# Kernel tuning notes

Hardware: AMD Instinct MI355X
Metric: run time of the kernel (lower is better)

Reference implementation:

```python
import jax, jax.numpy as jnp
import numpy as np

# ---- static config (mirrors ProposalLayerModule param) ----
FEAT_STRIDE = 16
PRE_NMS_TOPN = 6000
POST_NMS_TOPN = 300
NMS_THRESH = 0.7
MIN_SIZE = 16.0
NUM_ANCHORS = 9


def _generate_anchors():
    """Replicates generate_anchors(base_size=16, ratios=[0.5,1,2], scales=[8,16,32])."""
    base = np.array([0.0, 0.0, 15.0, 15.0])
    ratios = np.array([0.5, 1.0, 2.0])
    scales = np.array([8.0, 16.0, 32.0])
    w = base[2] - base[0] + 1.0
    h = base[3] - base[1] + 1.0
    xc = base[0] + 0.5 * (w - 1.0)
    yc = base[1] + 0.5 * (h - 1.0)
    size = w * h
    ws = np.round(np.sqrt(size / ratios))
    hs = np.round(ws * ratios)
    ratio_anchors = np.stack([xc - 0.5 * (ws - 1), yc - 0.5 * (hs - 1),
                              xc + 0.5 * (ws - 1), yc + 0.5 * (hs - 1)], axis=1)
    out = []
    for a in ratio_anchors:
        aw = a[2] - a[0] + 1.0
        ah = a[3] - a[1] + 1.0
        axc = a[0] + 0.5 * (aw - 1.0)
        ayc = a[1] + 0.5 * (ah - 1.0)
        ws2 = aw * scales
        hs2 = ah * scales
        out.append(np.stack([axc - 0.5 * (ws2 - 1), ayc - 0.5 * (hs2 - 1),
                             axc + 0.5 * (ws2 - 1), ayc + 0.5 * (hs2 - 1)], axis=1))
    return np.concatenate(out, axis=0).astype(np.float32)  # (9, 4)

_ANCHORS = _generate_anchors()


def _nms_keep(iou, valid, thresh):
    """Greedy NMS over score-sorted boxes. Returns boolean keep mask."""
    n = iou.shape[0]
    idx = jnp.arange(n)
    def body(i, keep):
        sup = keep[i] & (iou[i] > thresh) & (idx > i)
        return keep & jnp.logical_not(sup)
    return jax.lax.fori_loop(0, n, body, valid)


def setup_inputs() -> dict:
    key = jax.random.key(0)
    k1, k2 = jax.random.split(key)
    H, W = 128, 192
    scores = jax.random.normal(k1, (1, 2 * NUM_ANCHORS, H, W), dtype=jnp.float32)
    # small deltas so exp(dw), exp(dh) stay in a realistic range
    bbox_deltas = jax.random.normal(k2, (1, 4 * NUM_ANCHORS, H, W), dtype=jnp.float32) * 0.1
    im_info = jnp.array([H * FEAT_STRIDE, W * FEAT_STRIDE, 1.0], dtype=jnp.float32)
    return {"scores": scores, "bbox_deltas": bbox_deltas, "im_info": im_info}


def reference(scores, bbox_deltas, im_info):
    A = NUM_ANCHORS
    s = scores[0, A:]                      # (A, H, W) fg scores
    Hf, Wf = s.shape[1], s.shape[2]
    # shifts, matching torch.meshgrid default indexing='ij' (x-major flatten)
    shift_x = jnp.arange(Wf, dtype=jnp.float32) * FEAT_STRIDE
    shift_y = jnp.arange(Hf, dtype=jnp.float32) * FEAT_STRIDE
    sx, sy = jnp.meshgrid(shift_x, shift_y, indexing='ij')   # (W, H)
    shifts = jnp.stack([sx.ravel(), sy.ravel(), sx.ravel(), sy.ravel()], axis=1)  # (K,4)
    anchors = (jnp.asarray(_ANCHORS)[None, :, :] + shifts[:, None, :]).reshape(-1, 4)  # (K*A,4)

    deltas = jnp.transpose(bbox_deltas[0], (1, 2, 0)).reshape(-1, 4)  # (H*W*A,4)
    sc = jnp.transpose(s, (1, 2, 0)).reshape(-1)                      # (H*W*A,)

    # bbox_transform_inv
    widths = anchors[:, 2] - anchors[:, 0] + 1.0
    heights = anchors[:, 3] - anchors[:, 1] + 1.0
    ctr_x = anchors[:, 0] + 0.5 * widths
    ctr_y = anchors[:, 1] + 0.5 * heights
    dx, dy, dw, dh = deltas[:, 0], deltas[:, 1], deltas[:, 2], deltas[:, 3]
    pcx = dx * widths + ctr_x
    pcy = dy * heights + ctr_y
    pw = jnp.exp(dw) * widths
    ph = jnp.exp(dh) * heights
    x1 = pcx - 0.5 * pw
    y1 = pcy - 0.5 * ph
    x2 = pcx + 0.5 * pw
    y2 = pcy + 0.5 * ph

    # clip_boxes
    x1 = jnp.clip(x1, 0.0, im_info[1] - 1.0)
    x2 = jnp.clip(x2, 0.0, im_info[1] - 1.0)
    y1 = jnp.clip(y1, 0.0, im_info[0] - 1.0)
    y2 = jnp.clip(y2, 0.0, im_info[0] - 1.0)
    boxes = jnp.stack([x1, y1, x2, y2], axis=1)

    # _filter_boxes (as a mask, jit-friendly)
    ms = MIN_SIZE * im_info[2]
    valid = ((x2 - x1 + 1.0) >= ms) & ((y2 - y1 + 1.0) >= ms)
    masked_sc = jnp.where(valid, sc, -jnp.inf)

    # sort by score descending + pre_nms_topN
    top_s, top_i = jax.lax.top_k(masked_sc, PRE_NMS_TOPN)
    b = boxes[top_i]                       # (PRE, 4), score-sorted
    vld = jnp.isfinite(top_s)

    # torchvision-style IoU (no +1) + greedy NMS
    area = (b[:, 2] - b[:, 0]) * (b[:, 3] - b[:, 1])
    ix1 = jnp.maximum(b[:, None, 0], b[None, :, 0])
    iy1 = jnp.maximum(b[:, None, 1], b[None, :, 1])
    ix2 = jnp.minimum(b[:, None, 2], b[None, :, 2])
    iy2 = jnp.minimum(b[:, None, 3], b[None, :, 3])
    inter = jnp.clip(ix2 - ix1, 0.0) * jnp.clip(iy2 - iy1, 0.0)
    iou = inter / jnp.maximum(area[:, None] + area[None, :] - inter, 1e-9)
    keep = _nms_keep(iou, vld, NMS_THRESH)

    # first post_nms_topN kept boxes (fixed-size, zero-padded), prepend batch idx 0
    cum = jnp.cumsum(keep.astype(jnp.int32))
    pos = jnp.where(keep & (cum <= POST_NMS_TOPN), cum - 1, POST_NMS_TOPN)
    rows = jnp.concatenate([jnp.zeros((PRE_NMS_TOPN, 1), jnp.float32), b], axis=1)
    out = jnp.zeros((POST_NMS_TOPN + 1, 5), jnp.float32).at[pos].set(rows)[:POST_NMS_TOPN]
    return out
```

## Files before the change

### kernel.cpp

```cpp
#include <hip/hip_runtime.h>

#define NCELL 24576
#define NTOT  221184
#define NBIN13 8192
#define TOPN  6000
#define POSTN 300
#define NPADR 6016
#define NW    94
#define CW    8
#define NCHUNK 12
#define NCB   16
#define SLOT  1024
#define CAP2  (NCB*SLOT)

__global__ void decode_kernel(const float* __restrict__ scores,
                              const float* __restrict__ deltas,
                              const float* __restrict__ iminfo,
                              float4* __restrict__ boxes,
                              unsigned* __restrict__ skeys,
                              unsigned* __restrict__ ghist) {
#pragma clang fp contract(off)
    __shared__ unsigned lhist[NBIN13];
    int tid = threadIdx.x;
    for (int b = tid; b < NBIN13; b += 256) lhist[b] = 0u;
    __syncthreads();
    int c = blockIdx.x * blockDim.x + tid;
    if (c < NCELL) {
        const float AW[9] = {184.f,368.f,736.f,128.f,256.f,512.f, 88.f,176.f,352.f};
        const float AH[9] = { 96.f,192.f,384.f,128.f,256.f,512.f,176.f,352.f,704.f};
        float sx = (float)((c >> 7) << 4);
        float sy = (float)((c & 127) << 4);
        float imh = iminfo[0], imw = iminfo[1], ims = iminfo[2];
        float xhi = imw - 1.0f, yhi = imh - 1.0f;
        float ms = 16.0f * ims;
        float ctrx = sx + 8.0f, ctry = sy + 8.0f;
        const float* sbase = scores + 9 * NCELL + c;
        const float* dbase = deltas + c;
#pragma unroll
        for (int a = 0; a < 9; ++a) {
            float sc = sbase[a * NCELL];
            float dx = dbase[(4 * a + 0) * NCELL];
            float dy = dbase[(4 * a + 1) * NCELL];
            float dw = dbase[(4 * a + 2) * NCELL];
            float dh = dbase[(4 * a + 3) * NCELL];
            float pcx = dx * AW[a] + ctrx;
            float pcy = dy * AH[a] + ctry;
            float pw = expf(dw) * AW[a];
            float ph = expf(dh) * AH[a];
            float x1 = pcx - 0.5f * pw;
            float y1 = pcy - 0.5f * ph;
            float x2 = pcx + 0.5f * pw;
            float y2 = pcy + 0.5f * ph;
            x1 = fminf(fmaxf(x1, 0.0f), xhi);
            x2 = fminf(fmaxf(x2, 0.0f), xhi);
            y1 = fminf(fmaxf(y1, 0.0f), yhi);
            y2 = fminf(fmaxf(y2, 0.0f), yhi);
            bool valid = ((x2 - x1 + 1.0f) >= ms) && ((y2 - y1 + 1.0f) >= ms);
            unsigned u = __float_as_uint(sc);
            unsigned key = (u & 0x80000000u) ? ~u : (u | 0x80000000u);
            if (!valid) key = 0x007FFFFFu;
            boxes[a * NCELL + c] = make_float4(x1, y1, x2, y2);
            skeys[a * NCELL + c] = key;
            atomicAdd(&lhist[key >> 19], 1u);
        }
    }
    __syncthreads();
    for (int b = tid; b < NBIN13; b += 256) {
        unsigned v = lhist[b];
        if (v) atomicAdd(&ghist[b], v);
    }
}

__global__ __launch_bounds__(1024) void compactT_kernel(const unsigned* __restrict__ skeys,
                                                        const unsigned* __restrict__ ghist,
                                                        unsigned* __restrict__ meta16,
                                                        unsigned long long* __restrict__ cbuf) {
    __shared__ unsigned hist[NBIN13];
    __shared__ unsigned psum[1024];
    __shared__ unsigned csum[256];
    __shared__ unsigned sB, sAbove, sT, sCount;
    int tid = threadIdx.x, bid = blockIdx.x;
    {
        const uint4* gh4 = (const uint4*)ghist;
        uint4* h4 = (uint4*)hist;
        for (int q = tid; q < NBIN13 / 4; q += 1024) h4[q] = gh4[q];
    }
    if (tid == 0) sCount = 0u;
    __syncthreads();
    unsigned s = 0;
#pragma unroll
    for (int q = 0; q < 8; ++q) s += hist[tid * 8 + q];
    psum[tid] = s;
    __syncthreads();
    if (tid < 256)
        csum[tid] = psum[tid * 4] + psum[tid * 4 + 1] + psum[tid * 4 + 2] + psum[tid * 4 + 3];
    __syncthreads();
    if (tid < 64) {
        int lane = tid;
        unsigned c0 = csum[lane * 4 + 0], c1 = csum[lane * 4 + 1];
        unsigned c2 = csum[lane * 4 + 2], c3 = csum[lane * 4 + 3];
        unsigned ls = c0 + c1 + c2 + c3;
        unsigned v = ls;
#pragma unroll
        for (int o = 1; o < 64; o <<= 1) {
            unsigned t = __shfl_down(v, o, 64);
            if (lane + o < 64) v += t;
        }
        unsigned sufExcl = v - ls;
        unsigned a3 = sufExcl;
        unsigned a2 = a3 + c3;
        unsigned a1 = a2 + c2;
        unsigned a0 = a1 + c1;
        if (a0 < TOPN && a0 + c0 >= TOPN) { sB = lane * 4 + 0; sAbove = a0; }
        if (a1 < TOPN && a1 + c1 >= TOPN) { sB = lane * 4 + 1; sAbove = a1; }
        if (a2 < TOPN && a2 + c2 >= TOPN) { sB = lane * 4 + 2; sAbove = a2; }
        if (a3 < TOPN && a3 + c3 >= TOPN) { sB = lane * 4 + 3; sAbove = a3; }
    }
    __syncthreads();
    if (tid < 32) {
        unsigned B = sB, above = sAbove;
        unsigned h = hist[B * 32 + tid];
        unsigned v = h;
#pragma unroll
        for (int o = 1; o < 32; o <<= 1) {
            unsigned t = __shfl_down(v, o, 64);
            if (tid + o < 32) v += t;
        }
        unsigned sufExcl = v - h;
        unsigned ab = above + sufExcl;
        if (ab < TOPN && ab + h >= TOPN) sT = B * 32 + tid;
    }
    __syncthreads();
    unsigned T = sT;
    int base = bid * (NTOT / NCB);
    const uint4* s4b = (const uint4*)(skeys + base);
    for (int q = tid; q < (NTOT / NCB) / 4; q += 1024) {
        uint4 u = s4b[q];
        unsigned k4[4] = {u.x, u.y, u.z, u.w};
#pragma unroll
        for (int k = 0; k < 4; ++k) {
            if ((k4[k] >> 19) >= T) {
                unsigned lp = atomicAdd(&sCount, 1u);
                if (lp < SLOT) {
                    int m = base + 4 * q + k;
                    unsigned n = (unsigned)((m % NCELL) * 9 + (m / NCELL));
                    cbuf[(bid << 10) + lp] =
                        ((unsigned long long)k4[k] << 32) | (unsigned long long)(~n);
                }
            }
        }
    }
    __syncthreads();
    unsigned cnt = sCount; if (cnt > SLOT) cnt = SLOT;
    for (int e = cnt + tid; e < SLOT; e += 1024) cbuf[(bid << 10) + e] = 0ULL;
    if (tid == 0) meta16[bid] = cnt;
}

__global__ __launch_bounds__(256) void rankscatter_kernel(const unsigned long long* __restrict__ cbuf,
                                                          const unsigned* __restrict__ meta16,
                                                          const float4* __restrict__ boxes,
                                                          float4* __restrict__ sortedbox) {
    __shared__ unsigned long long jk[512];
    __shared__ unsigned scnt[NCB];
    int tid = threadIdx.x;
    if (tid < NCB) scnt[tid] = meta16[tid];
    __syncthreads();
    int i = blockIdx.x * 32 + (tid >> 3);
    int slice = tid & 7;
    unsigned long long ki = cbuf[i];
    unsigned cr = 0;
    for (int jt = 0; jt < CAP2 / 512; ++jt) {
        int b = jt >> 1;
        unsigned cb = scnt[b];
        if ((jt & 1) ? (cb <= 512u) : (cb == 0u)) continue;
        __syncthreads();
        for (int q = tid; q < 512; q += 256) jk[q] = cbuf[(jt << 9) + q];
        __syncthreads();
#pragma unroll 8
        for (int j = 0; j < 64; ++j) cr += (jk[slice + (j << 3)] > ki) ? 1u : 0u;
    }
    cr += __shfl_down(cr, 4, 8);
    cr += __shfl_down(cr, 2, 8);
    cr += __shfl_down(cr, 1, 8);
    if (slice == 0 && ki != 0ULL && cr < NPADR) {
        unsigned n = ~(unsigned)ki;
        unsigned m = (n % 9u) * (unsigned)NCELL + (n / 9u);
        sortedbox[cr] = boxes[m];
    }
}

__global__ __launch_bounds__(256) void matrix_kernel(const float4* __restrict__ sortedbox,
                                                     unsigned long long* __restrict__ rowr,
                                                     unsigned long long* __restrict__ diagw,
                                                     unsigned long long* __restrict__ diagT) {
#pragma clang fp contract(off)
    __shared__ float4 jb[256];
    __shared__ float  ja[256];
    int tid = threadIdx.x;
    int lane = tid & 63, wave = tid >> 6;
    int i0 = blockIdx.y << 6;
    int i = i0 + lane;
    int w = (blockIdx.x << 2) + wave;
    int jbase = blockIdx.x << 8;
    unsigned long long word = 0ULL;

    if (jbase + 255 > i0) {
        int jg = jbase + tid;
        float4 v = (jg < NPADR) ? sortedbox[jg] : make_float4(0.f, 0.f, 0.f, 0.f);
        jb[tid] = v;
        ja[tid] = (v.z - v.x) * (v.w - v.y);
        __syncthreads();
        if (w < NW && ((w << 6) + 63) > i) {
            float4 bi = sortedbox[i];
            float ai = (bi.z - bi.x) * (bi.w - bi.y);
            int jl0 = wave << 6;
            int jg0 = (w << 6);
#pragma unroll 8
            for (int j = 0; j < 64; ++j) {
                float4 bj = jb[jl0 + j];
                float aj = ja[jl0 + j];
                float iw = fminf(bi.z, bj.z) - fmaxf(bi.x, bj.x);
                float ih = fminf(bi.w, bj.w) - fmaxf(bi.y, bj.y);
                iw = fmaxf(iw, 0.0f);
                ih = fmaxf(ih, 0.0f);
                float inter = iw * ih;
                float denom = fmaxf(ai + aj - inter, 1e-9f);
                bool sup = (jg0 + j > i) && (inter / denom > 0.7f);
                word |= (unsigned long long)sup << j;
            }
        }
    }
    if (w < NW) {
        if (w >= (i >> 6))
            rowr[(size_t)i * NW + w] = word;
        if ((i >> 9) == (w >> 3) && w >= (i >> 6)) {
            unsigned long long col = 0ULL;
#pragma unroll
            for (int jbit = 0; jbit < 64; ++jbit) {
                unsigned long long m = __ballot((word >> jbit) & 1ULL);
                if (lane == jbit) col = m;
            }
            if (w == (i >> 6))
                diagT[((size_t)w << 6) + lane] = col;
            else
                diagw[((size_t)w << 9) + (i & 511)] = col;
        }
    }
}

__global__ __launch_bounds__(512) void scan_kernel(const unsigned long long* __restrict__ rowr,
                                                   const unsigned long long* __restrict__ diagw,
                                                   const unsigned long long* __restrict__ diagT,
                                                   const float4* __restrict__ sortedbox,
                                                   float* __restrict__ out) {
    __shared__ __align__(16) unsigned long long cblk[2][CW * 512];
    __shared__ __align__(16) unsigned long long ldsT[2][CW * 64];
    __shared__ unsigned long long gm[128];
    __shared__ int keptArr[POSTN];
    __shared__ int s_kept, s_done;
    int tid = threadIdx.x;
    int lane = tid & 63, wave = tid >> 6;

    if (tid < 128) gm[tid] = (tid == 93) ? ~((1ULL << 48) - 1) : 0ULL;
    if (tid == 0) { s_kept = 0; s_done = 0; }
    for (int pe = tid; pe < CW * 256; pe += 512) {
        int q = pe >> 8, r = (pe & 255) << 1;
        if (q > (r >> 6))
            *(ulonglong2*)&cblk[0][(q << 9) + r] =
                *(const ulonglong2*)&diagw[((size_t)q << 9) + r];
    }
    for (int pe = tid; pe < CW * 32; pe += 512) {
        int e = pe << 1;
        *(ulonglong2*)&ldsT[0][e] = *(const ulonglong2*)&diagT[e];
    }
    __syncthreads();

    int kA = 0;
    int kB = 0;
    for (int c = 0; c < NCHUNK; ++c) {
        int buf = c & 1, nbuf = buf ^ 1;
        int wbase = c * CW;
        if (wave == 0) {
            unsigned long long dgT[CW];
            unsigned long long gml[CW];
#pragma unroll
            for (int q = 0; q < CW; ++q) dgT[q] = ldsT[buf][(q << 6) + lane];
#pragma unroll
            for (int q = 0; q < CW; ++q) gml[q] = (wbase + q < NW) ? gm[wbase + q] : ~0ULL;
            unsigned long long lowmask = (1ULL << lane) - 1ULL;
            unsigned chunk_sup = 0;
            int kept = kB;
            int done = 0;
            int qmax = (NW - wbase < CW) ? (NW - wbase) : CW;
            for (int q = 0; q < qmax; ++q) {
                unsigned long long csup = __ballot((chunk_sup >> q) & 1u);
                unsigned long long live = ~(gml[q] | csup);
                if (wbase + q == NW - 1) live &= (1ULL << 48) - 1;
                if (!live) continue;
                bool alive = (live >> lane) & 1ULL;
                unsigned long long x = live;
                for (;;) {
                    bool sup = (dgT[q] & x & lowmask) != 0ULL;
                    unsigned long long xn = __ballot(alive && !sup);
                    if (xn == x) break;
                    x = xn;
                }
                unsigned long long kb = x;
                if (kb) {
                    int nk = __popcll(kb);
                    int myr = __popcll(kb & lowmask);
                    if (((kb >> lane) & 1ULL) && (kept + myr < POSTN))
                        keptArr[kept + myr] = ((wbase + q) << 6) + lane;
                    kept += nk;
                    if (kept >= POSTN) { kept = POSTN; done = 1; break; }
                    if (q < CW - 1) {
                        unsigned long long pr[CW];
#pragma unroll
                        for (int t = 0; t < CW; ++t)
                            pr[t] = cblk[buf][(t << 9) + (q << 6) + lane];
#pragma unroll
                        for (int t = 0; t < CW; ++t)
                            if (t > q && (pr[t] & kb)) chunk_sup |= 1u << t;
                    }
                }
            }
            if (lane == 0) { s_kept = kept; s_done = done; }
        } else {
            int t = tid - 64;
            if (c + 1 < NCHUNK) {
                int wb2 = wbase + CW;
                for (int pe = t; pe < CW * 256; pe += 448) {
                    int q = pe >> 8, r = (pe & 255) << 1;
                    if (q > (r >> 6)) {
                        ulonglong2 v = make_ulonglong2(0ULL, 0ULL);
                        if (wb2 + q < NW && wb2 + (r >> 6) < NW)
                            v = *(const ulonglong2*)&diagw[((size_t)(wb2 + q) << 9) + r];
                        *(ulonglong2*)&cblk[nbuf][(q << 9) + r] = v;
                    }
                }
                for (int pe = t; pe < CW * 32; pe += 448) {
                    int e = pe << 1, q = e >> 6;
                    ulonglong2 v = make_ulonglong2(0ULL, 0ULL);
                    if (wb2 + q < NW) v = *(const ulonglong2*)&diagT[((size_t)wb2 << 6) + e];
                    *(ulonglong2*)&ldsT[nbuf][e] = v;
                }
            }
            {
                int w2 = wbase + CW;
                int nw2 = NW - w2;
                int nr2 = kB - kA;
                if (c > 0 && nr2 > 0 && nw2 > 0) {
                    int npair = nw2 >> 1;
                    int tot = nr2 * npair;
                    for (int idx = t; idx < tot; idx += 448) {
                        int s = idx / npair, po = idx - s * npair;
                        int row = keptArr[kA + s];
                        ulonglong2 v = *(const ulonglong2*)&rowr[(size_t)row * NW + w2 + (po << 1)];
                        if (v.x) atomicOr(&gm[w2 + (po << 1)], v.x);
                        if (v.y) atomicOr(&gm[w2 + (po << 1) + 1], v.y);
                    }
                }
            }
        }
        __syncthreads();
        int keptNow = s_kept;
        bool fin = (s_done != 0) || (c == NCHUNK - 1);
        if (!fin && keptNow > kB) {
            int w1 = wbase + CW;
            int nw1 = NW - w1; if (nw1 > CW) nw1 = CW;
            int npair1 = nw1 >> 1;
            int po = tid & 3;
            for (int s = kB + (tid >> 2); s < keptNow; s += 128) {
                if (po < npair1) {
                    int row = keptArr[s];
                    ulonglong2 v = *(const ulonglong2*)&rowr[(size_t)row * NW + w1 + (po << 1)];
                    if (v.x) atomicOr(&gm[w1 + (po << 1)], v.x);
                    if (v.y) atomicOr(&gm[w1 + (po << 1) + 1], v.y);
                }
            }
        }
        kA = kB;
        kB = keptNow;
        if (fin) break;
        __syncthreads();
    }
    __syncthreads();

    int kept = s_kept;
    for (int k = tid; k < POSTN; k += 512) {
        float4 bb = make_float4(0.f, 0.f, 0.f, 0.f);
        if (k < kept) bb = sortedbox[keptArr[k]];
        out[k * 5 + 0] = 0.0f;
        out[k * 5 + 1] = bb.x;
        out[k * 5 + 2] = bb.y;
        out[k * 5 + 3] = bb.z;
        out[k * 5 + 4] = bb.w;
    }
}

extern "C" void kernel_launch(void* const* d_in, const int* in_sizes, int n_in,
                              void* d_out, int out_size, void* d_ws, size_t ws_size,
                              hipStream_t stream) {
    const float* scores = (const float*)d_in[0];
    const float* deltas = (const float*)d_in[1];
    const float* iminfo = (const float*)d_in[2];
    char* w = (char*)d_ws;
    float4*   boxes = (float4*)w;
    unsigned* skeys = (unsigned*)(w + 3538944);
    unsigned long long* rowr = (unsigned long long*)w;
    unsigned* meta16 = (unsigned*)(w + 4786176);
    unsigned long long* cbuf = (unsigned long long*)(w + 4786240);
    float4* sortedbox = (float4*)(w + 4917312);
    unsigned long long* diagw = (unsigned long long*)(w + 5013568);
    unsigned long long* diagT = (unsigned long long*)(w + 5398592);
    unsigned* ghist = (unsigned*)(w + 5446720);
    float* out = (float*)d_out;

    hipMemsetAsync(ghist, 0, NBIN13 * sizeof(unsigned), stream);
    decode_kernel<<<NCELL / 256, 256, 0, stream>>>(scores, deltas, iminfo, boxes, skeys, ghist);
    compactT_kernel<<<NCB, 1024, 0, stream>>>(skeys, ghist, meta16, cbuf);
    rankscatter_kernel<<<CAP2 / 32, 256, 0, stream>>>(cbuf, meta16, boxes, sortedbox);
    matrix_kernel<<<dim3(24, 94), 256, 0, stream>>>(sortedbox, rowr, diagw, diagT);
    scan_kernel<<<1, 512, 0, stream>>>(rowr, diagw, diagT, sortedbox, out);
}
```

Baseline: 135.7 us.

## Fuse decode and compaction into cooperative kernel; restructure NMS scan suppression merge

Merges the memset, decode and threshold/compaction kernels into one cooperative kernel that uses grid syncs. Each block recomputes the histogram threshold itself and writes candidates directly from registers via global per-slice atomic counters, so the skeys round-trip and two launches go away. Rankscatter now masks unfilled slots by count instead of relying on zero padding. In the NMS scan, the per-chunk atomicOr propagation of kept-row masks is replaced by wave 0 OR-reducing those rows inline at the start of each chunk, which removes a block-wide pass and one sync per chunk. The cost is grid-sync overhead, a cooperative launch limited to 96 blocks, redundant threshold work in every block, and a serial reload inside wave 0.

```diff
diff --git a/kernel.cpp b/kernel.cpp
--- a/kernel.cpp
+++ b/kernel.cpp
@@ -1,4 +1,5 @@
 #include <hip/hip_runtime.h>
+#include <hip/hip_cooperative_groups.h>
 
 #define NCELL 24576
 #define NTOT  221184
@@ -13,19 +14,26 @@
 #define SLOT  1024
 #define CAP2  (NCB*SLOT)
 
-__global__ void decode_kernel(const float* __restrict__ scores,
-                              const float* __restrict__ deltas,
-                              const float* __restrict__ iminfo,
-                              float4* __restrict__ boxes,
-                              unsigned* __restrict__ skeys,
-                              unsigned* __restrict__ ghist) {
+namespace cg = cooperative_groups;
+
+__global__ __launch_bounds__(256) void decode_compact_kernel(
+        const float* __restrict__ scores, const float* __restrict__ deltas,
+        const float* __restrict__ iminfo, float4* __restrict__ boxes,
+        unsigned* __restrict__ ghist, unsigned* __restrict__ gslice,
+        unsigned long long* __restrict__ cbuf) {
 #pragma clang fp contract(off)
+    cg::grid_group grid = cg::this_grid();
     __shared__ unsigned lhist[NBIN13];
+    __shared__ unsigned psum[256];
+    __shared__ unsigned sB, sAbove, sT;
     int tid = threadIdx.x;
+    int c = blockIdx.x * 256 + tid;
+    if (c < NBIN13) ghist[c] = 0u;
+    if (c < NCB) gslice[c] = 0u;
     for (int b = tid; b < NBIN13; b += 256) lhist[b] = 0u;
-    __syncthreads();
-    int c = blockIdx.x * blockDim.x + tid;
-    if (c < NCELL) {
+    grid.sync();
+    unsigned keyr[9];
+    {
         const float AW[9] = {184.f,368.f,736.f,128.f,256.f,512.f, 88.f,176.f,352.f};
         const float AH[9] = { 96.f,192.f,384.f,128.f,256.f,512.f,176.f,352.f,704.f};
         float sx = (float)((c >> 7) << 4);
@@ -60,7 +68,7 @@
             unsigned key = (u & 0x80000000u) ? ~u : (u | 0x80000000u);
             if (!valid) key = 0x007FFFFFu;
             boxes[a * NCELL + c] = make_float4(x1, y1, x2, y2);
-            skeys[a * NCELL + c] = key;
+            keyr[a] = key;
             atomicAdd(&lhist[key >> 19], 1u);
         }
     }
@@ -69,57 +77,42 @@
         unsigned v = lhist[b];
         if (v) atomicAdd(&ghist[b], v);
     }
-}
-
-__global__ __launch_bounds__(1024) void compactT_kernel(const unsigned* __restrict__ skeys,
-                                                        const unsigned* __restrict__ ghist,
-                                                        unsigned* __restrict__ meta16,
-                                                        unsigned long long* __restrict__ cbuf) {
-    __shared__ unsigned hist[NBIN13];
-    __shared__ unsigned psum[1024];
-    __shared__ unsigned csum[256];
-    __shared__ unsigned sB, sAbove, sT, sCount;
-    int tid = threadIdx.x, bid = blockIdx.x;
+    grid.sync();
     {
         const uint4* gh4 = (const uint4*)ghist;
-        uint4* h4 = (uint4*)hist;
-        for (int q = tid; q < NBIN13 / 4; q += 1024) h4[q] = gh4[q];
-    }
-    if (tid == 0) sCount = 0u;
+        uint4* h4 = (uint4*)lhist;
+        for (int q = tid; q < NBIN13 / 4; q += 256) h4[q] = gh4[q];
+    }
     __syncthreads();
     unsigned s = 0;
 #pragma unroll
-    for (int q = 0; q < 8; ++q) s += hist[tid * 8 + q];
+    for (int q = 0; q < 32; ++q) s += lhist[tid * 32 + q];
     psum[tid] = s;
     __syncthreads();
-    if (tid < 256)
-        csum[tid] = psum[tid * 4] + psum[tid * 4 + 1] + psum[tid * 4 + 2] + psum[tid * 4 + 3];
-    __syncthreads();
     if (tid < 64) {
-        int lane = tid;
-        unsigned c0 = csum[lane * 4 + 0], c1 = csum[lane * 4 + 1];
-        unsigned c2 = csum[lane * 4 + 2], c3 = csum[lane * 4 + 3];
+        unsigned c0 = psum[tid * 4 + 0], c1 = psum[tid * 4 + 1];
+        unsigned c2 = psum[tid * 4 + 2], c3 = psum[tid * 4 + 3];
         unsigned ls = c0 + c1 + c2 + c3;
         unsigned v = ls;
 #pragma unroll
         for (int o = 1; o < 64; o <<= 1) {
             unsigned t = __shfl_down(v, o, 64);
-            if (lane + o < 64) v += t;
+            if (tid + o < 64) v += t;
         }
         unsigned sufExcl = v - ls;
         unsigned a3 = sufExcl;
         unsigned a2 = a3 + c3;
         unsigned a1 = a2 + c2;
         unsigned a0 = a1 + c1;
-        if (a0 < TOPN && a0 + c0 >= TOPN) { sB = lane * 4 + 0; sAbove = a0; }
-        if (a1 < TOPN && a1 + c1 >= TOPN) { sB = lane * 4 + 1; sAbove = a1; }
-        if (a2 < TOPN && a2 + c2 >= TOPN) { sB = lane * 4 + 2; sAbove = a2; }
-        if (a3 < TOPN && a3 + c3 >= TOPN) { sB = lane * 4 + 3; sAbove = a3; }
+        if (a0 < TOPN && a0 + c0 >= TOPN) { sB = tid * 4 + 0; sAbove = a0; }
+        if (a1 < TOPN && a1 + c1 >= TOPN) { sB = tid * 4 + 1; sAbove = a1; }
+        if (a2 < TOPN && a2 + c2 >= TOPN) { sB = tid * 4 + 2; sAbove = a2; }
+        if (a3 < TOPN && a3 + c3 >= TOPN) { sB = tid * 4 + 3; sAbove = a3; }
     }
     __syncthreads();
     if (tid < 32) {
         unsigned B = sB, above = sAbove;
-        unsigned h = hist[B * 32 + tid];
+        unsigned h = lhist[B * 32 + tid];
         unsigned v = h;
 #pragma unroll
         for (int o = 1; o < 32; o <<= 1) {
@@ -132,28 +125,20 @@
     }
     __syncthreads();
     unsigned T = sT;
-    int base = bid * (NTOT / NCB);
-    const uint4* s4b = (const uint4*)(skeys + base);
-    for (int q = tid; q < (NTOT / NCB) / 4; q += 1024) {
-        uint4 u = s4b[q];
-        unsigned k4[4] = {u.x, u.y, u.z, u.w};
-#pragma unroll
-        for (int k = 0; k < 4; ++k) {
-            if ((k4[k] >> 19) >= T) {
-                unsigned lp = atomicAdd(&sCount, 1u);
-                if (lp < SLOT) {
-                    int m = base + 4 * q + k;
-                    unsigned n = (unsigned)((m % NCELL) * 9 + (m / NCELL));
-                    cbuf[(bid << 10) + lp] =
-                        ((unsigned long long)k4[k] << 32) | (unsigned long long)(~n);
-                }
-            }
-        }
-    }
-    __syncthreads();
-    unsigned cnt = sCount; if (cnt > SLOT) cnt = SLOT;
-    for (int e = cnt + tid; e < SLOT; e += 1024) cbuf[(bid << 10) + e] = 0ULL;
-    if (tid == 0) meta16[bid] = cnt;
+#pragma unroll
+    for (int a = 0; a < 9; ++a) {
+        unsigned key = keyr[a];
+        if ((key >> 19) >= T) {
+            int m = a * NCELL + c;
+            int slice = m / (NTOT / NCB);
+            unsigned lp = atomicAdd(&gslice[slice], 1u);
+            if (lp < SLOT) {
+                unsigned n = (unsigned)(c * 9 + a);
+                cbuf[((unsigned)slice << 10) + lp] =
+                    ((unsigned long long)key << 32) | (unsigned long long)(~n);
+            }
+        }
+    }
 }
 
 __global__ __launch_bounds__(256) void rankscatter_kernel(const unsigned long long* __restrict__ cbuf,
@@ -163,18 +148,24 @@
     __shared__ unsigned long long jk[512];
     __shared__ unsigned scnt[NCB];
     int tid = threadIdx.x;
-    if (tid < NCB) scnt[tid] = meta16[tid];
+    if (tid < NCB) {
+        unsigned m = meta16[tid];
+        scnt[tid] = (m > SLOT) ? SLOT : m;
+    }
     __syncthreads();
     int i = blockIdx.x * 32 + (tid >> 3);
     int slice = tid & 7;
-    unsigned long long ki = cbuf[i];
+    unsigned long long ki = ((unsigned)(i & 1023) < scnt[i >> 10]) ? cbuf[i] : 0ULL;
     unsigned cr = 0;
     for (int jt = 0; jt < CAP2 / 512; ++jt) {
         int b = jt >> 1;
         unsigned cb = scnt[b];
         if ((jt & 1) ? (cb <= 512u) : (cb == 0u)) continue;
         __syncthreads();
-        for (int q = tid; q < 512; q += 256) jk[q] = cbuf[(jt << 9) + q];
+        for (int q = tid; q < 512; q += 256) {
+            unsigned p = ((unsigned)(jt & 1) << 9) + (unsigned)q;
+            jk[q] = (p < cb) ? cbuf[(jt << 9) + q] : 0ULL;
+        }
         __syncthreads();
 #pragma unroll 8
         for (int j = 0; j < 64; ++j) cr += (jk[slice + (j << 3)] > ki) ? 1u : 0u;
@@ -281,6 +272,16 @@
         int buf = c & 1, nbuf = buf ^ 1;
         int wbase = c * CW;
         if (wave == 0) {
+            unsigned long long inl = 0ULL;
+            {
+                int q = lane & 7;
+                if (wbase + q < NW)
+                    for (int s = kA + (lane >> 3); s < kB; s += 8)
+                        inl |= rowr[(size_t)keptArr[s] * NW + wbase + q];
+                inl |= __shfl_xor(inl, 8, 64);
+                inl |= __shfl_xor(inl, 16, 64);
+                inl |= __shfl_xor(inl, 32, 64);
+            }
             unsigned long long dgT[CW];
             unsigned long long gml[CW];
 #pragma unroll
@@ -294,7 +295,7 @@
             int qmax = (NW - wbase < CW) ? (NW - wbase) : CW;
             for (int q = 0; q < qmax; ++q) {
                 unsigned long long csup = __ballot((chunk_sup >> q) & 1u);
-                unsigned long long live = ~(gml[q] | csup);
+                unsigned long long live = ~(gml[q] | __shfl(inl, q, 64) | csup);
                 if (wbase + q == NW - 1) live &= (1ULL << 48) - 1;
                 if (!live) continue;
                 bool alive = (live >> lane) & 1ULL;
@@ -363,26 +364,9 @@
             }
         }
         __syncthreads();
-        int keptNow = s_kept;
-        bool fin = (s_done != 0) || (c == NCHUNK - 1);
-        if (!fin && keptNow > kB) {
-            int w1 = wbase + CW;
-            int nw1 = NW - w1; if (nw1 > CW) nw1 = CW;
-            int npair1 = nw1 >> 1;
-            int po = tid & 3;
-            for (int s = kB + (tid >> 2); s < keptNow; s += 128) {
-                if (po < npair1) {
-                    int row = keptArr[s];
-                    ulonglong2 v = *(const ulonglong2*)&rowr[(size_t)row * NW + w1 + (po << 1)];
-                    if (v.x) atomicOr(&gm[w1 + (po << 1)], v.x);
-                    if (v.y) atomicOr(&gm[w1 + (po << 1) + 1], v.y);
-                }
-            }
-        }
         kA = kB;
-        kB = keptNow;
-        if (fin) break;
-        __syncthreads();
+        kB = s_kept;
+        if (s_done != 0 || c == NCHUNK - 1) break;
     }
     __syncthreads();
 
@@ -406,9 +390,8 @@
     const float* iminfo = (const float*)d_in[2];
     char* w = (char*)d_ws;
     float4*   boxes = (float4*)w;
-    unsigned* skeys = (unsigned*)(w + 3538944);
     unsigned long long* rowr = (unsigned long long*)w;
-    unsigned* meta16 = (unsigned*)(w + 4786176);
+    unsigned* gslice = (unsigned*)(w + 4786176);
     unsigned long long* cbuf = (unsigned long long*)(w + 4786240);
     float4* sortedbox = (float4*)(w + 4917312);
     unsigned long long* diagw = (unsigned long long*)(w + 5013568);
@@ -416,10 +399,11 @@
     unsigned* ghist = (unsigned*)(w + 5446720);
     float* out = (float*)d_out;
 
-    hipMemsetAsync(ghist, 0, NBIN13 * sizeof(unsigned), stream);
-    decode_kernel<<<NCELL / 256, 256, 0, stream>>>(scores, deltas, iminfo, boxes, skeys, ghist);
-    compactT_kernel<<<NCB, 1024, 0, stream>>>(skeys, ghist, meta16, cbuf);
-    rankscatter_kernel<<<CAP2 / 32, 256, 0, stream>>>(cbuf, meta16, boxes, sortedbox);
+    void* kargs[] = { (void*)&scores, (void*)&deltas, (void*)&iminfo, (void*)&boxes,
+                      (void*)&ghist, (void*)&gslice, (void*)&cbuf };
+    hipLaunchCooperativeKernel(reinterpret_cast<void*>(&decode_compact_kernel),
+                               dim3(96), dim3(256), kargs, 0u, stream);
+    rankscatter_kernel<<<CAP2 / 32, 256, 0, stream>>>(cbuf, gslice, boxes, sortedbox);
     matrix_kernel<<<dim3(24, 94), 256, 0, stream>>>(sortedbox, rowr, diagw, diagT);
     scan_kernel<<<1, 512, 0, stream>>>(rowr, diagw, diagT, sortedbox, out);
 }
```

Result: slower. 252.3 us (+86.0%).
